# Kernel tuning notes

Hardware: AMD Instinct MI355X
Metric: run time of the kernel (lower is better)

The kernel has to match this reference:

```python
import jax, jax.numpy as jnp
import numpy as np


def hard_sigmoid(x):
    return jnp.clip((x + 1.0) * 0.5, 0.0, 1.0)


def setup_inputs() -> dict:
    key = jax.random.key(0)
    k1, k2 = jax.random.split(key)
    N, D, F = 1048576, 128, 128
    inputs = jax.random.normal(k1, (N, D), dtype=jnp.float32)
    # lecun_normal init: std = 1/sqrt(fan_in)
    weight = jax.random.normal(k2, (D, F), dtype=jnp.float32) * (1.0 / np.sqrt(D))
    return {"inputs": inputs, "weight": weight, "seed": 0, "is_training": 1}


def reference(inputs, weight, seed, is_training):
    rng = jax.random.key(seed)
    if is_training:
        p = hard_sigmoid(weight)  # P(w_bin = +1)
        w_bin = jax.random.bernoulli(rng, p=p).astype(inputs.dtype) * 2.0 - 1.0
    else:
        w_bin = jnp.where(weight > 0, 1.0, -1.0).astype(inputs.dtype)
    # [N, D] @ [D, F] -> [N, F]
    return jnp.dot(inputs, w_bin)
```

## Files before the change

kernel.cpp:

```cpp
#include <hip/hip_runtime.h>
#include <stdint.h>


typedef _Float16 half8 __attribute__((ext_vector_type(8)));
typedef float f32x4 __attribute__((ext_vector_type(4)));

__device__ __forceinline__ uint32_t rotl32(uint32_t x, int n) {
    return (x << n) | (x >> (32 - n));
}

__device__ __forceinline__ void threefry2x32(uint32_t k0, uint32_t k1,
                                             uint32_t x0, uint32_t x1,
                                             uint32_t& o0, uint32_t& o1) {
    const uint32_t ks0 = k0, ks1 = k1, ks2 = 0x1BD11BDAu ^ k0 ^ k1;
    x0 += ks0; x1 += ks1;
#define TF_ROUND(r) { x0 += x1; x1 = rotl32(x1, (r)); x1 ^= x0; }
    TF_ROUND(13) TF_ROUND(15) TF_ROUND(26) TF_ROUND(6)
    x0 += ks1; x1 += ks2 + 1u;
    TF_ROUND(17) TF_ROUND(29) TF_ROUND(16) TF_ROUND(24)
    x0 += ks2; x1 += ks0 + 2u;
    TF_ROUND(13) TF_ROUND(15) TF_ROUND(26) TF_ROUND(6)
    x0 += ks0; x1 += ks1 + 3u;
    TF_ROUND(17) TF_ROUND(29) TF_ROUND(16) TF_ROUND(24)
    x0 += ks1; x1 += ks2 + 4u;
    TF_ROUND(13) TF_ROUND(15) TF_ROUND(26) TF_ROUND(6)
    x0 += ks2; x1 += ks0 + 5u;
#undef TF_ROUND
    o0 = x0; o1 = x1;
}

__global__ void binarize_kernel(const float* __restrict__ weight,
                                const int* __restrict__ seed_p,
                                const int* __restrict__ train_p,
                                unsigned short* __restrict__ bfrag) {
    const int i = blockIdx.x * 256 + threadIdx.x;
    const uint32_t seed_lo = (uint32_t)(*seed_p);
    const int training = *train_p;
    const float w = weight[i];

    unsigned short sign_bits;
    if (training) {
        uint32_t o0, o1;
        threefry2x32(0u, seed_lo, 0u, (uint32_t)i, o0, o1);
        const uint32_t bits = o0 ^ o1;
        const float u = __uint_as_float((bits >> 9) | 0x3F800000u) - 1.0f;
        float p = (w + 1.0f) * 0.5f;
        p = fminf(fmaxf(p, 0.0f), 1.0f);
        sign_bits = (u < p) ? 0x3C00u : 0xBC00u;
    } else {
        sign_bits = (w > 0.0f) ? 0x3C00u : 0xBC00u;
    }

    const int k = i >> 7, n = i & 127;
    const int tile = n >> 4, kstep = k >> 5, q = (k >> 3) & 3, j = k & 7;
    const int lane = q * 16 + (n & 15);
    bfrag[((tile * 4 + kstep) * 64 + lane) * 8 + j] = sign_bits;
}

__global__ __launch_bounds__(256, 4)
void gemm_bin_kernel(const float* __restrict__ A,
                     const unsigned short* __restrict__ bfrag,
                     float* __restrict__ out,
                     int nstrips) {
    __shared__ unsigned short ldsB[16384];
    {
        const uint4* src = (const uint4*)bfrag;
        uint4* dst = (uint4*)ldsB;
        const int t = threadIdx.x;
#pragma unroll
        for (int i = 0; i < 8; ++i) dst[t + i * 256] = src[t + i * 256];
    }
    __syncthreads();

    const int lane = threadIdx.x & 63;
    const int wv = threadIdx.x >> 6;
    const int m = lane & 15;
    const int q = lane >> 4;

    for (int s = blockIdx.x; s < nstrips; s += gridDim.x) {
        const int64_t base_row = (int64_t)s * 64 + wv * 16;
        const float* arow = A + (base_row + m) * 128 + q * 8;

        float4 fbuf[8];
#pragma unroll
        for (int kk = 0; kk < 4; ++kk) {
            fbuf[2 * kk]     = *(const float4*)(arow + kk * 32);
            fbuf[2 * kk + 1] = *(const float4*)(arow + kk * 32 + 4);
        }
        half8 afr[4];
#pragma unroll
        for (int kk = 0; kk < 4; ++kk) {
            afr[kk][0] = (_Float16)fbuf[2 * kk].x;
            afr[kk][1] = (_Float16)fbuf[2 * kk].y;
            afr[kk][2] = (_Float16)fbuf[2 * kk].z;
            afr[kk][3] = (_Float16)fbuf[2 * kk].w;
            afr[kk][4] = (_Float16)fbuf[2 * kk + 1].x;
            afr[kk][5] = (_Float16)fbuf[2 * kk + 1].y;
            afr[kk][6] = (_Float16)fbuf[2 * kk + 1].z;
            afr[kk][7] = (_Float16)fbuf[2 * kk + 1].w;
        }

        float* orow = out + (base_row + q * 4) * 128 + m;
#pragma unroll
        for (int t = 0; t < 8; ++t) {
            f32x4 acc = {0.f, 0.f, 0.f, 0.f};
#pragma unroll
            for (int kk = 0; kk < 4; ++kk) {
                const half8 bfr = *(const half8*)(&ldsB[((t * 4 + kk) * 64 + lane) * 8]);
                acc = __builtin_amdgcn_mfma_f32_16x16x32_f16(afr[kk], bfr, acc, 0, 0, 0);
            }
#pragma unroll
            for (int r = 0; r < 4; ++r) orow[r * 128 + t * 16] = acc[r];
        }
    }
}

extern "C" void kernel_launch(void* const* d_in, const int* in_sizes, int n_in,
                              void* d_out, int out_size, void* d_ws, size_t ws_size,
                              hipStream_t stream) {
    const float* A = (const float*)d_in[0];
    const float* W = (const float*)d_in[1];
    const int* seed = (const int*)d_in[2];
    const int* train = (const int*)d_in[3];
    float* out = (float*)d_out;
    unsigned short* bfrag = (unsigned short*)d_ws;

    const int N = in_sizes[0] / 128;
    const int nstrips = N / 64;

    binarize_kernel<<<64, 256, 0, stream>>>(W, seed, train, bfrag);

    int grid = 4096;
    if (grid > nstrips) grid = nstrips;
    gemm_bin_kernel<<<grid, 256, 0, stream>>>(A, bfrag, out, nstrips);
}
```

Before: 945.5 us.

## Prefetch next A strip, swap MFMA operands for vector stores, shrink grid

Issues the global loads for the next strip's A rows before computing the current strip, so load latency overlaps the MFMAs. The MFMA operands are swapped so each lane holds four consecutive output columns, which allows a single float4 store per tile in place of four scattered scalar stores. The grid drops from 4096 to 1024 blocks so each block loops over more strips and the prefetch has work to overlap with, at the cost of more registers per thread.

```diff
diff --git a/kernel.cpp b/kernel.cpp
--- a/kernel.cpp
+++ b/kernel.cpp
@@ -70,23 +70,27 @@
 #pragma unroll
         for (int i = 0; i < 8; ++i) dst[t + i * 256] = src[t + i * 256];
     }
-    __syncthreads();
 
     const int lane = threadIdx.x & 63;
     const int wv = threadIdx.x >> 6;
     const int m = lane & 15;
     const int q = lane >> 4;
 
-    for (int s = blockIdx.x; s < nstrips; s += gridDim.x) {
-        const int64_t base_row = (int64_t)s * 64 + wv * 16;
-        const float* arow = A + (base_row + m) * 128 + q * 8;
+    int s = (int)blockIdx.x;
+    const int sstep = (int)gridDim.x;
 
-        float4 fbuf[8];
+    float4 fbuf[8];
+    if (s < nstrips) {
+        const float* arow = A + ((int64_t)s * 64 + wv * 16 + m) * 128 + q * 8;
 #pragma unroll
         for (int kk = 0; kk < 4; ++kk) {
             fbuf[2 * kk]     = *(const float4*)(arow + kk * 32);
             fbuf[2 * kk + 1] = *(const float4*)(arow + kk * 32 + 4);
         }
+    }
+    __syncthreads();
+
+    while (s < nstrips) {
         half8 afr[4];
 #pragma unroll
         for (int kk = 0; kk < 4; ++kk) {
@@ -100,18 +104,30 @@
             afr[kk][7] = (_Float16)fbuf[2 * kk + 1].w;
         }
 
-        float* orow = out + (base_row + q * 4) * 128 + m;
+        const int snext = s + sstep;
+        if (snext < nstrips) {
+            const float* arow = A + ((int64_t)snext * 64 + wv * 16 + m) * 128 + q * 8;
 #pragma unroll
-        for (int t = 0; t < 8; ++t) {
+            for (int kk = 0; kk < 4; ++kk) {
+                fbuf[2 * kk]     = *(const float4*)(arow + kk * 32);
+                fbuf[2 * kk + 1] = *(const float4*)(arow + kk * 32 + 4);
+            }
+        }
+
+        float* orow = out + ((int64_t)s * 64 + wv * 16 + m) * 128 + q * 4;
+#pragma unroll
+        for (int tt = 0; tt < 8; ++tt) {
             f32x4 acc = {0.f, 0.f, 0.f, 0.f};
 #pragma unroll
             for (int kk = 0; kk < 4; ++kk) {
-                const half8 bfr = *(const half8*)(&ldsB[((t * 4 + kk) * 64 + lane) * 8]);
-                acc = __builtin_amdgcn_mfma_f32_16x16x32_f16(afr[kk], bfr, acc, 0, 0, 0);
+                const half8 wfr = *(const half8*)(&ldsB[((tt * 4 + kk) * 64 + lane) * 8]);
+                acc = __builtin_amdgcn_mfma_f32_16x16x32_f16(wfr, afr[kk], acc, 0, 0, 0);
             }
-#pragma unroll
-            for (int r = 0; r < 4; ++r) orow[r * 128 + t * 16] = acc[r];
+            float4 o;
+            o.x = acc[0]; o.y = acc[1]; o.z = acc[2]; o.w = acc[3];
+            *(float4*)(orow + tt * 16) = o;
         }
+        s = snext;
     }
 }
 
@@ -130,7 +146,7 @@
 
     binarize_kernel<<<64, 256, 0, stream>>>(W, seed, train, bfrag);
 
-    int grid = 4096;
+    int grid = 1024;
     if (grid > nstrips) grid = nstrips;
     gemm_bin_kernel<<<grid, 256, 0, stream>>>(A, bfrag, out, nstrips);
 }
```

Measured after the change: 1.012 ms. +7.1%, slower.
